# Performance work log

Measured on AMD Instinct MI355X. Metric: run time of the kernel, lower is better.

Reference implementation:

```python
import jax, jax.numpy as jnp
import numpy as np

EPS = 1e-5

def _ln(x, g, b):
    mu = jnp.mean(x, axis=-1, keepdims=True)
    var = jnp.var(x, axis=-1, keepdims=True)
    return (x - mu) * jax.lax.rsqrt(var + EPS) * g + b

def setup_inputs() -> dict:
    B, N, D, H = 8, 1024, 1024, 16
    hid = 4 * D
    key = jax.random.key(0)
    ks = jax.random.split(key, 16)
    s = lambda fan_in: 1.0 / np.sqrt(fan_in)
    return {
        "x": jax.random.normal(ks[0], (B, N, D), jnp.float32),
        "ln1_g": jnp.ones((D,), jnp.float32),
        "ln1_b": jnp.zeros((D,), jnp.float32),
        "qkv_w": jax.random.normal(ks[1], (D, 3 * D), jnp.float32) * s(D),
        "qkv_b": jnp.zeros((3 * D,), jnp.float32),
        "proj_w": jax.random.normal(ks[2], (D, D), jnp.float32) * s(D),
        "proj_b": jnp.zeros((D,), jnp.float32),
        "ls1_g": jnp.full((D,), 1e-5, jnp.float32),
        "ln2_g": jnp.ones((D,), jnp.float32),
        "ln2_b": jnp.zeros((D,), jnp.float32),
        "fc1_w": jax.random.normal(ks[3], (D, hid), jnp.float32) * s(D),
        "fc1_b": jnp.zeros((hid,), jnp.float32),
        "fc2_w": jax.random.normal(ks[4], (hid, D), jnp.float32) * s(hid),
        "fc2_b": jnp.zeros((D,), jnp.float32),
        "ls2_g": jnp.full((D,), 1e-5, jnp.float32),
    }

def reference(x, ln1_g, ln1_b, qkv_w, qkv_b, proj_w, proj_b, ls1_g,
              ln2_g, ln2_b, fc1_w, fc1_b, fc2_w, fc2_b, ls2_g):
    B, N, D = x.shape
    H = 16
    hd = D // H
    scale = hd ** -0.5
    # --- attention branch (pre-norm) ---
    h = _ln(x, ln1_g, ln1_b)
    qkv = h @ qkv_w + qkv_b                      # [B,N,3D]
    q, k, v = jnp.split(qkv, 3, axis=-1)
    reshape = lambda t: t.reshape(B, N, H, hd).transpose(0, 2, 1, 3)  # [B,H,N,hd]
    q, k, v = reshape(q), reshape(k), reshape(v)
    attn = jax.nn.softmax(jnp.einsum('bhnd,bhmd->bhnm', q, k) * scale, axis=-1)
    o = jnp.einsum('bhnm,bhmd->bhnd', attn, v)
    o = o.transpose(0, 2, 1, 3).reshape(B, N, D)
    o = o @ proj_w + proj_b
    x = x + ls1_g * o
    # --- MLP branch (pre-norm) ---
    h = _ln(x, ln2_g, ln2_b)
    h = jax.nn.gelu(h @ fc1_w + fc1_b, approximate=False)
    h = h @ fc2_w + fc2_b
    x = x + ls2_g * h
    return x
```

## Files before the change

### kernel.cpp

```cpp
#include <hip/hip_runtime.h>
#include <hip/hip_bf16.h>
#include <cstdint>

using u16 = unsigned short;
using u8 = unsigned char;
typedef __attribute__((ext_vector_type(8))) short bf16x8;
typedef __attribute__((ext_vector_type(4))) float f32x4;
typedef __attribute__((ext_vector_type(16))) float f32x16;
typedef __attribute__((ext_vector_type(8))) int i32x8;
typedef __attribute__((ext_vector_type(4))) u16 u16x4;

#define MFMA_BF16(a, b, c) __builtin_amdgcn_mfma_f32_16x16x32_bf16((a), (b), (c), 0, 0, 0)
#define MFMA_FP8(a, b, c) \
  __builtin_amdgcn_mfma_scale_f32_32x32x64_f8f6f4((a), (b), (c), 0, 0, 0, 0x7f7f7f7f, 0, 0x7f7f7f7f)

__device__ __forceinline__ u16 f2bf(float f) {
  __hip_bfloat16 h = __float2bfloat16(f);
  return __builtin_bit_cast(u16, h);
}

__device__ __forceinline__ u8 f2fp8(float a) {
  int r = __builtin_amdgcn_cvt_pk_fp8_f32(a, a, 0, false);
  return (u8)(r & 0xff);
}

__device__ __forceinline__ uint32_t f2fp8x4(float a, float b, float c, float d) {
  int r = __builtin_amdgcn_cvt_pk_fp8_f32(a, b, 0, false);
  r = __builtin_amdgcn_cvt_pk_fp8_f32(c, d, r, true);
  return (uint32_t)r;
}

__device__ __forceinline__ void gl_lds16(const void* gsrc, void* ldst) {
  __builtin_amdgcn_global_load_lds(
      (__attribute__((address_space(1))) void*)const_cast<void*>(gsrc),
      (__attribute__((address_space(3))) void*)ldst, 16, 0, 0);
}

__global__ __launch_bounds__(256) void transpose_conv8(const float* __restrict__ src,
                                                       u8* __restrict__ dst, int K, int N) {
  __shared__ float t[32][33];
  const int bx = blockIdx.x, by = blockIdx.y;
  const int tid = threadIdx.x;
  const int r = tid >> 3, c = (tid & 7) * 4;
  const float4 v = *(const float4*)&src[(size_t)(by * 32 + r) * N + bx * 32 + c];
  t[r][c] = v.x; t[r][c + 1] = v.y; t[r][c + 2] = v.z; t[r][c + 3] = v.w;
  __syncthreads();
  uint32_t o = f2fp8x4(t[c][r], t[c + 1][r], t[c + 2][r], t[c + 3][r]);
  *(uint32_t*)&dst[(size_t)(bx * 32 + r) * K + by * 32 + c] = o;
}

__global__ __launch_bounds__(256) void transpose_v(const u16* __restrict__ qkv, u16* __restrict__ dst) {
  __shared__ u16 t[32][40];
  const int bx = blockIdx.x;
  const int by = blockIdx.y;
  const int bh = blockIdx.z;
  const int b = bh >> 4, h = bh & 15;
  const int tid = threadIdx.x;
  const int r = tid >> 3, c = (tid & 7) * 4;
  u16x4 v = *(const u16x4*)&qkv[(size_t)(b * 1024 + by * 32 + r) * 3072 + 2048 + h * 64 + bx * 32 + c];
  t[r][c] = v.x; t[r][c + 1] = v.y; t[r][c + 2] = v.z; t[r][c + 3] = v.w;
  __syncthreads();
  u16x4 o = {t[c][r], t[c + 1][r], t[c + 2][r], t[c + 3][r]};
  *(u16x4*)&dst[(size_t)bh * 65536 + (size_t)(bx * 32 + r) * 1024 + by * 32 + c] = o;
}

__global__ __launch_bounds__(256) void ln_kernel(const float* __restrict__ x, const float* __restrict__ g,
                                                 const float* __restrict__ b, u8* __restrict__ out) {
  const int row = blockIdx.x, tid = threadIdx.x;
  const float* xr = x + (size_t)row * 1024;
  float4 v = *(const float4*)&xr[tid * 4];
  float s = v.x + v.y + v.z + v.w;
  float s2 = v.x * v.x + v.y * v.y + v.z * v.z + v.w * v.w;
#pragma unroll
  for (int off = 32; off; off >>= 1) { s += __shfl_xor(s, off); s2 += __shfl_xor(s2, off); }
  __shared__ float ps[4], ps2[4];
  const int wave = tid >> 6;
  if ((tid & 63) == 0) { ps[wave] = s; ps2[wave] = s2; }
  __syncthreads();
  s = ps[0] + ps[1] + ps[2] + ps[3];
  s2 = ps2[0] + ps2[1] + ps2[2] + ps2[3];
  const float mu = s * (1.0f / 1024.0f);
  const float var = s2 * (1.0f / 1024.0f) - mu * mu;
  const float rs = rsqrtf(var + 1e-5f);
  float4 gv = *(const float4*)&g[tid * 4];
  float4 bv = *(const float4*)&b[tid * 4];
  uint32_t o = f2fp8x4((v.x - mu) * rs * gv.x + bv.x, (v.y - mu) * rs * gv.y + bv.y,
                       (v.z - mu) * rs * gv.z + bv.z, (v.w - mu) * rs * gv.w + bv.w);
  *(uint32_t*)&out[(size_t)row * 1024 + tid * 4] = o;
}

__device__ __forceinline__ i32x8 ld_frag8(const u8* S, int row, int kk, int lk, int sw) {
  const int c0 = kk * 4 + lk * 2;
  const u8* rp = S + row * 128;
  int4 lo = *(const int4*)(rp + ((c0 ^ sw) * 16));
  int4 hi = *(const int4*)(rp + (((c0 + 1) ^ sw) * 16));
  i32x8 r = {lo.x, lo.y, lo.z, lo.w, hi.x, hi.y, hi.z, hi.w};
  return r;
}

template <int EPI>
__global__ __launch_bounds__(256, 3) void gemm_f8(const u8* __restrict__ A, const u8* __restrict__ Bt,
                                                  const float* __restrict__ bias, const float* __restrict__ xres,
                                                  const float* __restrict__ ls, float* __restrict__ outf,
                                                  u16* __restrict__ outh, u8* __restrict__ out8,
                                                  int M, int N, int K) {
  __shared__ __attribute__((aligned(16))) u8 As[128 * 128];
  __shared__ __attribute__((aligned(16))) u8 Bs[128 * 128];
  const int tid = threadIdx.x;
  const int w = tid >> 6, l = tid & 63;
  const int wr = w >> 1, wc = w & 1;
  const int l31 = l & 31, lk = l >> 5, sw = l & 7;
  const int bm = blockIdx.x, bn = blockIdx.y;

  f32x16 acc[2][2];
#pragma unroll
  for (int mi = 0; mi < 2; mi++)
#pragma unroll
    for (int ni = 0; ni < 2; ni++)
#pragma unroll
      for (int r = 0; r < 16; r++) acc[mi][ni][r] = 0.f;

  const int srow = w * 8 + (l >> 3);
  const int schunk = ((l & 7) ^ (l >> 3)) * 16;
  const u8* Ag = A + (size_t)(bm * 128 + srow) * K + schunk;
  const u8* Bg = Bt + (size_t)(bn * 128 + srow) * K + schunk;
  u8* Asw = &As[w * 1024];
  u8* Bsw = &Bs[w * 1024];
  const size_t row32K = (size_t)32 * K;

  for (int kt = 0; kt < K; kt += 128) {
    __syncthreads();
#pragma unroll
    for (int i = 0; i < 4; i++) gl_lds16(Ag + i * row32K + kt, Asw + i * 4096);
#pragma unroll
    for (int i = 0; i < 4; i++) gl_lds16(Bg + i * row32K + kt, Bsw + i * 4096);
    __syncthreads();
#pragma unroll
    for (int kk = 0; kk < 2; kk++) {
      i32x8 af[2], bf[2];
#pragma unroll
      for (int mi = 0; mi < 2; mi++) af[mi] = ld_frag8(As, wr * 64 + mi * 32 + l31, kk, lk, sw);
#pragma unroll
      for (int ni = 0; ni < 2; ni++) bf[ni] = ld_frag8(Bs, wc * 64 + ni * 32 + l31, kk, lk, sw);
#pragma unroll
      for (int mi = 0; mi < 2; mi++)
#pragma unroll
        for (int ni = 0; ni < 2; ni++) acc[mi][ni] = MFMA_FP8(af[mi], bf[ni], acc[mi][ni]);
    }
  }

  const int row0 = bm * 128 + wr * 64 + lk * 4;
  const int col0 = bn * 128 + wc * 64 + l31;
#pragma unroll
  for (int mi = 0; mi < 2; mi++)
#pragma unroll
    for (int ni = 0; ni < 2; ni++)
#pragma unroll
      for (int reg = 0; reg < 16; reg++) {
        const int r = row0 + mi * 32 + (reg & 3) + 8 * (reg >> 2);
        const int c = col0 + ni * 32;
        float v = acc[mi][ni][reg];
        if constexpr (EPI == 0) {
          outh[(size_t)r * N + c] = f2bf(v + bias[c]);
        } else if constexpr (EPI == 1) {
          const size_t idx = (size_t)r * N + c;
          outf[idx] = xres[idx] + ls[c] * (v + bias[c]);
        } else if constexpr (EPI == 2) {
          v += bias[c];
          out8[(size_t)r * N + c] = f2fp8(0.5f * v * (1.0f + erff(v * 0.70710678118654752f)));
        } else {
          const size_t idx = (size_t)r * N + c;
          outf[idx] += ls[c] * (v + bias[c]);
        }
      }
}

__global__ __launch_bounds__(256, 3) void attn_kernel(const u16* __restrict__ qkv, const u16* __restrict__ vt,
                                                      u8* __restrict__ o) {
  __shared__ __attribute__((aligned(16))) u16 Ks[128 * 64];
  __shared__ __attribute__((aligned(16))) u16 Vs[64 * 128];
  __shared__ __attribute__((aligned(16))) u16 PQ[4 * 16 * 128];
  u16* Qs = PQ;
  const int tid = threadIdx.x;
  const int wave = tid >> 6, lane = tid & 63;
  const int lrow = lane & 15, lhi = lane >> 4;
  const int qt = blockIdx.x;
  const int bh = blockIdx.y;
  const int b = bh >> 4, h = bh & 15;
  const int swz8 = (lane & 7) ^ (lane >> 3);
  const int swz16 = (lane & 15) ^ (wave * 4 + (lane >> 4));
  const float SC = 0.18033688011f;

  {
    const u16* gq = qkv + (size_t)(b * 1024 + qt * 64 + wave * 8 + (lane >> 3)) * 3072 + h * 64 + swz8 * 8;
    gl_lds16(gq, &Qs[(wave * 8) * 64]);
    gl_lds16(gq + (size_t)32 * 3072, &Qs[(32 + wave * 8) * 64]);
  }
  __syncthreads();
  const int pq0 = (lhi ^ (lrow & 7)) * 8;
  bf16x8 qf0 = *(const bf16x8*)&Qs[(wave * 16 + lrow) * 64 + pq0];
  bf16x8 qf1 = *(const bf16x8*)&Qs[(wave * 16 + lrow) * 64 + (pq0 ^ 32)];

  float m_ = -1e30f, l_ = 0.f;
  f32x4 oa[4];
  f32x4 zero = {0.f, 0.f, 0.f, 0.f};
#pragma unroll
  for (int i = 0; i < 4; i++) oa[i] = zero;

  const u16* kg = qkv + (size_t)(b * 1024 + wave * 8 + (lane >> 3)) * 3072 + 1024 + h * 64 + swz8 * 8;
  const u16* vg = vt + (size_t)bh * 65536 + (size_t)(wave * 4 + (lane >> 4)) * 1024 + swz16 * 8;

  for (int kt = 0; kt < 1024; kt += 128) {
    __syncthreads();
#pragma unroll
    for (int i = 0; i < 4; i++) gl_lds16(kg + (size_t)(kt + i * 32) * 3072, &Ks[(i * 32 + wave * 8) * 64]);
#pragma unroll
    for (int i = 0; i < 4; i++) gl_lds16(vg + (size_t)(i * 16) * 1024 + kt, &Vs[(i * 16 + wave * 4) * 128]);
    __syncthreads();

    f32x4 sf[8];
#pragma unroll
    for (int n = 0; n < 8; n++) sf[n] = zero;
#pragma unroll
    for (int n = 0; n < 8; n++) {
      bf16x8 kf0 = *(const bf16x8*)&Ks[(n * 16 + lrow) * 64 + pq0];
      bf16x8 kf1 = *(const bf16x8*)&Ks[(n * 16 + lrow) * 64 + (pq0 ^ 32)];
      sf[n] = MFMA_BF16(kf0, qf0, sf[n]);
      sf[n] = MFMA_BF16(kf1, qf1, sf[n]);
    }

    float tn[8];
#pragma unroll
    for (int n = 0; n < 8; n++)
      tn[n] = fmaxf(fmaxf(sf[n][0], sf[n][1]), fmaxf(sf[n][2], sf[n][3]));
    float tm = fmaxf(fmaxf(fmaxf(tn[0], tn[1]), fmaxf(tn[2], tn[3])),
                     fmaxf(fmaxf(tn[4], tn[5]), fmaxf(tn[6], tn[7])));
    tm = fmaxf(tm, __shfl_xor(tm, 16));
    tm = fmaxf(tm, __shfl_xor(tm, 32));
    tm *= SC;

    if (!__all(tm <= m_ + 8.0f)) {
      const float mn = fmaxf(m_, tm);
      const float al = exp2f(m_ - mn);
      m_ = mn;
      l_ *= al;
#pragma unroll
      for (int i = 0; i < 4; i++) {
        const float a = __shfl(al, lhi * 4 + i);
        oa[0][i] *= a; oa[1][i] *= a; oa[2][i] *= a; oa[3][i] *= a;
      }
    }

    float rsv[4] = {0.f, 0.f, 0.f, 0.f};
#pragma unroll
    for (int n = 0; n < 8; n++) {
      u16x4 pk;
#pragma unroll
      for (int i = 0; i < 4; i++) {
        const float p = exp2f(sf[n][i] * SC - m_);
        rsv[i] += p;
        pk[i] = f2bf(p);
      }
      const int c = 2 * n + (lhi >> 1);
      *(u16x4*)&PQ[wave * 2048 + lrow * 128 + ((c ^ lrow) * 8) + (lhi & 1) * 4] = pk;
    }
    float rs = (rsv[0] + rsv[1]) + (rsv[2] + rsv[3]);
    rs += __shfl_xor(rs, 16);
    rs += __shfl_xor(rs, 32);
    l_ += rs;

#pragma unroll
    for (int ks = 0; ks < 4; ks++) {
      bf16x8 pf = *(const bf16x8*)&PQ[wave * 2048 + lrow * 128 + (((ks * 4 + lhi) ^ lrow) * 8)];
#pragma unroll
      for (int n2 = 0; n2 < 4; n2++) {
        bf16x8 vf = *(const bf16x8*)&Vs[(n2 * 16 + lrow) * 128 + (((ks * 4 + lhi) ^ lrow) * 8)];
        oa[n2] = MFMA_BF16(pf, vf, oa[n2]);
      }
    }
  }

  float lq[4];
#pragma unroll
  for (int i = 0; i < 4; i++) lq[i] = 1.0f / __shfl(l_, lhi * 4 + i);
#pragma unroll
  for (int n2 = 0; n2 < 4; n2++)
#pragma unroll
    for (int i = 0; i < 4; i++) {
      const int tok = qt * 64 + wave * 16 + lhi * 4 + i;
      o[(size_t)(b * 1024 + tok) * 1024 + h * 64 + n2 * 16 + lrow] = f2fp8(oa[n2][i] * lq[i]);
    }
}

extern "C" void kernel_launch(void* const* d_in, const int* in_sizes, int n_in, void* d_out, int out_size,
                              void* d_ws, size_t ws_size, hipStream_t stream) {
  const float* x = (const float*)d_in[0];
  const float* ln1_g = (const float*)d_in[1];
  const float* ln1_b = (const float*)d_in[2];
  const float* qkv_w = (const float*)d_in[3];
  const float* qkv_b = (const float*)d_in[4];
  const float* proj_w = (const float*)d_in[5];
  const float* proj_b = (const float*)d_in[6];
  const float* ls1_g = (const float*)d_in[7];
  const float* ln2_g = (const float*)d_in[8];
  const float* ln2_b = (const float*)d_in[9];
  const float* fc1_w = (const float*)d_in[10];
  const float* fc1_b = (const float*)d_in[11];
  const float* fc2_w = (const float*)d_in[12];
  const float* fc2_b = (const float*)d_in[13];
  const float* ls2_g = (const float*)d_in[14];
  float* out = (float*)d_out;

  u8* p = (u8*)d_ws;
  u8* wq8 = p;  p += (size_t)3072 * 1024;
  u8* wp8 = p;  p += (size_t)1024 * 1024;
  u8* wf18 = p; p += (size_t)4096 * 1024;
  u8* wf28 = p; p += (size_t)1024 * 4096;
  u8* hbuf8 = p; p += (size_t)8192 * 1024;
  u16* qkvb = (u16*)p; p += (size_t)8192 * 3072 * 2;
  u16* vtb = (u16*)p;  p += (size_t)128 * 64 * 1024 * 2;
  u8* ob8 = p;  p += (size_t)8192 * 1024;
  u8* hid8 = (u8*)qkvb;

  transpose_conv8<<<dim3(96, 32), 256, 0, stream>>>(qkv_w, wq8, 1024, 3072);
  transpose_conv8<<<dim3(32, 32), 256, 0, stream>>>(proj_w, wp8, 1024, 1024);
  transpose_conv8<<<dim3(128, 32), 256, 0, stream>>>(fc1_w, wf18, 1024, 4096);
  transpose_conv8<<<dim3(32, 128), 256, 0, stream>>>(fc2_w, wf28, 4096, 1024);

  ln_kernel<<<8192, 256, 0, stream>>>(x, ln1_g, ln1_b, hbuf8);
  gemm_f8<0><<<dim3(64, 24), 256, 0, stream>>>(hbuf8, wq8, qkv_b, nullptr, nullptr, nullptr, qkvb, nullptr,
                                               8192, 3072, 1024);
  transpose_v<<<dim3(2, 32, 128), 256, 0, stream>>>(qkvb, vtb);
  attn_kernel<<<dim3(16, 128), 256, 0, stream>>>(qkvb, vtb, ob8);
  gemm_f8<1><<<dim3(64, 8), 256, 0, stream>>>(ob8, wp8, proj_b, x, ls1_g, out, nullptr, nullptr,
                                              8192, 1024, 1024);
  ln_kernel<<<8192, 256, 0, stream>>>(out, ln2_g, ln2_b, hbuf8);
  gemm_f8<2><<<dim3(64, 32), 256, 0, stream>>>(hbuf8, wf18, fc1_b, nullptr, nullptr, nullptr, nullptr, hid8,
                                               8192, 4096, 1024);
  gemm_f8<3><<<dim3(64, 8), 256, 0, stream>>>(hid8, wf28, fc2_b, nullptr, ls2_g, out, nullptr, nullptr,
                                              8192, 1024, 4096);
}
```

Before: 284.7 us.

## Double-buffer K/V tiles in attention and fold softmax scale into Q

The attention kernel now keeps two LDS buffers for K and V and issues the global-to-LDS loads for the next key tile before computing on the current one, with explicit vmcnt waits and raw barriers in place of full syncthreads. This is meant to hide load latency behind the MFMA and softmax work. The softmax scale (log2e/sqrt(hd)) is moved into the QKV GEMM epilogue for the Q columns, which removes a multiply per score. The bigger LDS footprint lowers the launch bound from 3 to 2 blocks per SM, so occupancy may drop.

```diff
diff --git a/kernel.cpp b/kernel.cpp
--- a/kernel.cpp
+++ b/kernel.cpp
@@ -161,7 +161,9 @@
         const int c = col0 + ni * 32;
         float v = acc[mi][ni][reg];
         if constexpr (EPI == 0) {
-          outh[(size_t)r * N + c] = f2bf(v + bias[c]);
+          float ov = v + bias[c];
+          if (c < 1024) ov *= 0.18033688011f;
+          outh[(size_t)r * N + c] = f2bf(ov);
         } else if constexpr (EPI == 1) {
           const size_t idx = (size_t)r * N + c;
           outf[idx] = xres[idx] + ls[c] * (v + bias[c]);
@@ -175,11 +177,11 @@
       }
 }
 
-__global__ __launch_bounds__(256, 3) void attn_kernel(const u16* __restrict__ qkv, const u16* __restrict__ vt,
+__global__ __launch_bounds__(256, 2) void attn_kernel(const u16* __restrict__ qkv, const u16* __restrict__ vt,
                                                       u8* __restrict__ o) {
-  __shared__ __attribute__((aligned(16))) u16 Ks[128 * 64];
-  __shared__ __attribute__((aligned(16))) u16 Vs[64 * 128];
-  __shared__ __attribute__((aligned(16))) u16 PQ[4 * 16 * 128];
+  __shared__ __attribute__((aligned(16))) u16 Ks[2][128 * 64];
+  __shared__ __attribute__((aligned(16))) u16 Vs[2][64 * 128];
+  __shared__ __attribute__((aligned(16))) u16 PQ[4 * 2048];
   u16* Qs = PQ;
   const int tid = threadIdx.x;
   const int wave = tid >> 6, lane = tid & 63;
@@ -189,17 +191,32 @@
   const int b = bh >> 4, h = bh & 15;
   const int swz8 = (lane & 7) ^ (lane >> 3);
   const int swz16 = (lane & 15) ^ (wave * 4 + (lane >> 4));
-  const float SC = 0.18033688011f;
+
+  const u16* kg = qkv + (size_t)(b * 1024 + wave * 8 + (lane >> 3)) * 3072 + 1024 + h * 64 + swz8 * 8;
+  const u16* vg = vt + (size_t)bh * 65536 + (size_t)(wave * 4 + (lane >> 4)) * 1024 + swz16 * 8;
+
+  auto stageKV = [&](int tk, int bb) {
+#pragma unroll
+    for (int i = 0; i < 4; i++)
+      gl_lds16(kg + (size_t)(tk * 128 + i * 32) * 3072, &Ks[bb][(i * 32 + wave * 8) * 64]);
+#pragma unroll
+    for (int i = 0; i < 4; i++)
+      gl_lds16(vg + (size_t)(i * 16) * 1024 + tk * 128, &Vs[bb][(i * 16 + wave * 4) * 128]);
+  };
 
   {
     const u16* gq = qkv + (size_t)(b * 1024 + qt * 64 + wave * 8 + (lane >> 3)) * 3072 + h * 64 + swz8 * 8;
     gl_lds16(gq, &Qs[(wave * 8) * 64]);
     gl_lds16(gq + (size_t)32 * 3072, &Qs[(32 + wave * 8) * 64]);
   }
-  __syncthreads();
+  stageKV(0, 0);
+  asm volatile("s_waitcnt vmcnt(8)" ::: "memory");
+  __builtin_amdgcn_s_barrier();
   const int pq0 = (lhi ^ (lrow & 7)) * 8;
   bf16x8 qf0 = *(const bf16x8*)&Qs[(wave * 16 + lrow) * 64 + pq0];
   bf16x8 qf1 = *(const bf16x8*)&Qs[(wave * 16 + lrow) * 64 + (pq0 ^ 32)];
+  asm volatile("s_waitcnt lgkmcnt(0)" ::: "memory");
+  __builtin_amdgcn_sched_barrier(0);
 
   float m_ = -1e30f, l_ = 0.f;
   f32x4 oa[4];
@@ -207,24 +224,24 @@
 #pragma unroll
   for (int i = 0; i < 4; i++) oa[i] = zero;
 
-  const u16* kg = qkv + (size_t)(b * 1024 + wave * 8 + (lane >> 3)) * 3072 + 1024 + h * 64 + swz8 * 8;
-  const u16* vg = vt + (size_t)bh * 65536 + (size_t)(wave * 4 + (lane >> 4)) * 1024 + swz16 * 8;
-
-  for (int kt = 0; kt < 1024; kt += 128) {
-    __syncthreads();
-#pragma unroll
-    for (int i = 0; i < 4; i++) gl_lds16(kg + (size_t)(kt + i * 32) * 3072, &Ks[(i * 32 + wave * 8) * 64]);
-#pragma unroll
-    for (int i = 0; i < 4; i++) gl_lds16(vg + (size_t)(i * 16) * 1024 + kt, &Vs[(i * 16 + wave * 4) * 128]);
-    __syncthreads();
+  for (int t = 0; t < 8; ++t) {
+    const int cur = t & 1;
+    __builtin_amdgcn_s_barrier();
+    if (t < 7) {
+      stageKV(t + 1, cur ^ 1);
+      asm volatile("s_waitcnt vmcnt(8)" ::: "memory");
+    } else {
+      asm volatile("s_waitcnt vmcnt(0)" ::: "memory");
+    }
+    __builtin_amdgcn_s_barrier();
 
     f32x4 sf[8];
 #pragma unroll
     for (int n = 0; n < 8; n++) sf[n] = zero;
 #pragma unroll
     for (int n = 0; n < 8; n++) {
-      bf16x8 kf0 = *(const bf16x8*)&Ks[(n * 16 + lrow) * 64 + pq0];
-      bf16x8 kf1 = *(const bf16x8*)&Ks[(n * 16 + lrow) * 64 + (pq0 ^ 32)];
+      bf16x8 kf0 = *(const bf16x8*)&Ks[cur][(n * 16 + lrow) * 64 + pq0];
+      bf16x8 kf1 = *(const bf16x8*)&Ks[cur][(n * 16 + lrow) * 64 + (pq0 ^ 32)];
       sf[n] = MFMA_BF16(kf0, qf0, sf[n]);
       sf[n] = MFMA_BF16(kf1, qf1, sf[n]);
     }
@@ -237,7 +254,6 @@
                      fmaxf(fmaxf(tn[4], tn[5]), fmaxf(tn[6], tn[7])));
     tm = fmaxf(tm, __shfl_xor(tm, 16));
     tm = fmaxf(tm, __shfl_xor(tm, 32));
-    tm *= SC;
 
     if (!__all(tm <= m_ + 8.0f)) {
       const float mn = fmaxf(m_, tm);
@@ -257,7 +273,7 @@
       u16x4 pk;
 #pragma unroll
       for (int i = 0; i < 4; i++) {
-        const float p = exp2f(sf[n][i] * SC - m_);
+        const float p = exp2f(sf[n][i] - m_);
         rsv[i] += p;
         pk[i] = f2bf(p);
       }
@@ -274,7 +290,7 @@
       bf16x8 pf = *(const bf16x8*)&PQ[wave * 2048 + lrow * 128 + (((ks * 4 + lhi) ^ lrow) * 8)];
 #pragma unroll
       for (int n2 = 0; n2 < 4; n2++) {
-        bf16x8 vf = *(const bf16x8*)&Vs[(n2 * 16 + lrow) * 128 + (((ks * 4 + lhi) ^ lrow) * 8)];
+        bf16x8 vf = *(const bf16x8*)&Vs[cur][(n2 * 16 + lrow) * 128 + (((ks * 4 + lhi) ^ lrow) * 8)];
         oa[n2] = MFMA_BF16(pf, vf, oa[n2]);
       }
     }
```

Result: slower. 296.5 us (+4.1%).
